# Kernel optimization log

Measured on AMD Instinct MI355X. Metric: run time of the kernel, lower is better.

The kernel has to match this reference:

```python
import jax, jax.numpy as jnp
import numpy as np

N = 50000   # nodes
E = 800000  # edges
F = 64      # num_node_features
H = 64      # hidden_channels
NB = 3      # num_blocks
G = 64      # graphs in batch
C = 10      # num_classes
EPS = 1e-5  # BatchNorm eps


def setup_inputs() -> dict:
    key = jax.random.key(0)
    ks = jax.random.split(key, 24)
    x = jax.random.normal(ks[0], (N, F), dtype=jnp.float32)
    edge_index = jax.random.randint(ks[1], (2, E), 0, N, dtype=jnp.int64)
    batch = jnp.sort(jax.random.randint(ks[2], (N,), 0, G, dtype=jnp.int64))
    s = 0.05
    inp = {
        "x": x, "edge_index": edge_index, "batch": batch,
        "pre_w": jax.random.normal(ks[3], (F, H)) * s,
        "pre_b": jnp.zeros((H,), jnp.float32),
        # stacked per-block params (blocks are structurally identical)
        "blk_prelu1": jnp.full((NB,), 0.25, jnp.float32),
        "blk_bn_gamma": jnp.ones((NB, H), jnp.float32),
        "blk_bn_beta": jnp.zeros((NB, H), jnp.float32),
        "blk_w1": jax.random.normal(ks[4], (NB, H, 2 * H)) * s,
        "blk_b1": jnp.zeros((NB, 2 * H), jnp.float32),
        "blk_prelu2": jnp.full((NB,), 0.25, jnp.float32),
        "blk_w2": jax.random.normal(ks[5], (NB, 2 * H, H)) * s,
        "blk_b2": jnp.zeros((NB, H), jnp.float32),
        "post_bn_gamma": jnp.ones((H,), jnp.float32),
        "post_bn_beta": jnp.zeros((H,), jnp.float32),
        "fc1_w": jax.random.normal(ks[6], (H, 4 * H)) * s,
        "fc1_b": jnp.zeros((4 * H,), jnp.float32),
        "post_prelu": jnp.asarray(0.25, jnp.float32),
        "fc2_w": jax.random.normal(ks[7], (4 * H, C)) * s,
        "fc2_b": jnp.zeros((C,), jnp.float32),
    }
    return inp


def _prelu(x, a):
    return jnp.where(x >= 0, x, a * x)


def _batchnorm(x, gamma, beta):
    # training-mode BN over the node dimension (biased variance), as in torch
    mean = jnp.mean(x, axis=0)
    var = jnp.var(x, axis=0)
    return (x - mean) * jax.lax.rsqrt(var + EPS) * gamma + beta


def _gcn_conv(x, W, bias, src, dst):
    # PyG GCNConv: linear transform, then D^-1/2 (A+I) D^-1/2 aggregation, then bias.
    h = x @ W                                   # [N, out]
    deg = jax.ops.segment_sum(jnp.ones((E,), h.dtype), dst, num_segments=N) + 1.0
    dinv = jax.lax.rsqrt(deg)                   # [N]
    norm = dinv[src] * dinv[dst]                # [E]
    agg = jax.ops.segment_sum(h[src] * norm[:, None], dst, num_segments=N)
    agg = agg + h * (dinv * dinv)[:, None]      # self-loop contribution
    return agg + bias


def reference(x, edge_index, batch, pre_w, pre_b,
              blk_prelu1, blk_bn_gamma, blk_bn_beta, blk_w1, blk_b1,
              blk_prelu2, blk_w2, blk_b2,
              post_bn_gamma, post_bn_beta, fc1_w, fc1_b, post_prelu, fc2_w, fc2_b):
    src, dst = edge_index[0], edge_index[1]
    h = x @ pre_w + pre_b                       # [N, H]
    for i in range(NB):
        h = _prelu(h, blk_prelu1[i])
        h = _batchnorm(h, blk_bn_gamma[i], blk_bn_beta[i])
        h = _gcn_conv(h, blk_w1[i], blk_b1[i], src, dst)   # [N, 2H]
        h = _prelu(h, blk_prelu2[i])
        h = _gcn_conv(h, blk_w2[i], blk_b2[i], src, dst)   # [N, H]
    # global mean pool per graph
    sums = jax.ops.segment_sum(h, batch, num_segments=G)   # [G, H]
    cnts = jax.ops.segment_sum(jnp.ones((N,), h.dtype), batch, num_segments=G)
    pooled = sums / jnp.maximum(cnts, 1.0)[:, None]
    out = _batchnorm(pooled, post_bn_gamma, post_bn_beta)
    out = out @ fc1_w + fc1_b
    out = _prelu(out, post_prelu)
    # dropout with p=0.0 is identity
    out = out @ fc2_w + fc2_b                   # [G, C]
    return out
```

## Files before the change

kernel.cpp:

```cpp
#include <hip/hip_runtime.h>
#include <hip/hip_fp16.h>

#define NN 50000
#define NE 800000
#define NG 64
#define NC 10
#define BN_EPS 1e-5f
#define NSB 196

typedef __attribute__((ext_vector_type(2))) _Float16 h2v;
typedef __attribute__((ext_vector_type(8))) _Float16 f16x8;
typedef __attribute__((ext_vector_type(4))) float f32x4;

__device__ __forceinline__ float2 up2(unsigned u) {
    __half2 h = *reinterpret_cast<__half2*>(&u);
    return __half22float2(h);
}
__device__ __forceinline__ unsigned pk2(float a, float b) {
    __half2 h = __floats2half2_rn(a, b);
    return *reinterpret_cast<unsigned*>(&h);
}
__device__ __forceinline__ float fdot2u(unsigned a, unsigned b, float c) {
    return __builtin_amdgcn_fdot2(__builtin_bit_cast(h2v, a), __builtin_bit_cast(h2v, b), c, false);
}


__global__ void deg_count_kernel(const int* __restrict__ dst, int* __restrict__ deg,
                                 unsigned short* __restrict__ pos16) {
    int e = blockIdx.x * blockDim.x + threadIdx.x;
    if (e < NE) {
        int d = __builtin_nontemporal_load(&dst[e]);
        unsigned short p = (unsigned short)atomicAdd(&deg[d], 1);
        __builtin_nontemporal_store(p, &pos16[e]);
    }
}

__global__ __launch_bounds__(256) void block_sum_kernel(const int* __restrict__ deg,
                                                        int* __restrict__ bsum) {
    int b = blockIdx.x, t = threadIdx.x;
    int n = b * 256 + t;
    int v = (n < NN) ? deg[n] : 0;
    __shared__ int red[256];
    red[t] = v;
    __syncthreads();
    for (int off = 128; off > 0; off >>= 1) {
        if (t < off) red[t] += red[t + off];
        __syncthreads();
    }
    if (t == 0) bsum[b] = red[0];
}

__global__ __launch_bounds__(256) void bsum_scan_kernel(const int* __restrict__ bsum,
                                                        int* __restrict__ boff) {
    __shared__ int s[256];
    int t = threadIdx.x;
    int v = (t < NSB) ? bsum[t] : 0;
    s[t] = v;
    __syncthreads();
    for (int off = 1; off < 256; off <<= 1) {
        int cur = s[t];
        int add = (t >= off) ? s[t - off] : 0;
        __syncthreads();
        s[t] = cur + add;
        __syncthreads();
    }
    if (t < NSB) boff[t] = s[t] - v;
}

__global__ __launch_bounds__(256) void csr_setup_kernel(const int* __restrict__ deg,
                                                        const int* __restrict__ boff,
                                                        int* __restrict__ row_off,
                                                        float* __restrict__ dinv,
                                                        float* __restrict__ rdeg) {
    int b = blockIdx.x, t = threadIdx.x;
    int n = b * 256 + t;
    int v = (n < NN) ? deg[n] : 0;
    __shared__ int s[256];
    s[t] = v;
    __syncthreads();
    for (int off = 1; off < 256; off <<= 1) {
        int cur = s[t];
        int add = (t >= off) ? s[t - off] : 0;
        __syncthreads();
        s[t] = cur + add;
        __syncthreads();
    }
    int excl = s[t] - v + boff[b];
    if (n < NN) {
        row_off[n] = excl;
        float d = (float)v + 1.0f;
        dinv[n] = rsqrtf(d);
        rdeg[n] = sqrtf(d);
    }
    if (n == NN - 1) row_off[NN] = NE;
}

__global__ void scatter_pass_kernel(const int* __restrict__ src, const int* __restrict__ dst,
                                    const unsigned short* __restrict__ pos16,
                                    const int* __restrict__ row_off,
                                    int* __restrict__ csr_src, int d0, int d1) {
    int e = blockIdx.x * blockDim.x + threadIdx.x;
    if (e >= NE) return;
    int d = __builtin_nontemporal_load(&dst[e]);
    if (d < d0 || d >= d1) return;
    int s = __builtin_nontemporal_load(&src[e]);
    int p = (int)__builtin_nontemporal_load(&pos16[e]);
    csr_src[row_off[d] + p] = s;
}

__global__ void arow_kernel(const int* __restrict__ row_off, const int* __restrict__ csr_src,
                            const float* __restrict__ dinv, float* __restrict__ arow) {
    int n = blockIdx.x * 256 + threadIdx.x;
    if (n >= NN) return;
    float dv = dinv[n];
    float s = dv;
    int e0 = row_off[n], e1 = row_off[n + 1];
    for (int i = e0; i < e1; ++i) s += dinv[csr_src[i]];
    arow[n] = dv * s;
}


__global__ __launch_bounds__(256) void bn_stats_kernel(const __half* __restrict__ h,
                                                       const float* __restrict__ rdeg,
                                                       const float* __restrict__ alpha_p,
                                                       float* __restrict__ stats) {
    float alpha = alpha_p[0];
    int tid = threadIdx.x;
    int c4 = (tid & 15) * 4;
    int rg = tid >> 4;
    float sx = 0, sy = 0, sz = 0, sw = 0;
    float qx = 0, qy = 0, qz = 0, qw = 0;
    for (int n = blockIdx.x * 16 + rg; n < NN; n += gridDim.x * 16) {
        float rd = rdeg[n];
        uint2 u = *(const uint2*)&h[(size_t)n * 64 + c4];
        float2 lo = up2(u.x), hi = up2(u.y);
        float a = lo.x >= 0.f ? lo.x : alpha * lo.x;
        float b = lo.y >= 0.f ? lo.y : alpha * lo.y;
        float c = hi.x >= 0.f ? hi.x : alpha * hi.x;
        float d = hi.y >= 0.f ? hi.y : alpha * hi.y;
        a *= rd; b *= rd; c *= rd; d *= rd;
        sx += a; sy += b; sz += c; sw += d;
        qx += a * a; qy += b * b; qz += c * c; qw += d * d;
    }
    __shared__ float ls[256 * 8];
    float* p = &ls[tid * 8];
    p[0] = sx; p[1] = sy; p[2] = sz; p[3] = sw;
    p[4] = qx; p[5] = qy; p[6] = qz; p[7] = qw;
    __syncthreads();
    if (tid < 128) {
        int cidx = tid >> 3;
        int j = tid & 7;
        float acc = 0.f;
        for (int r = 0; r < 16; ++r) acc += ls[(r * 16 + cidx) * 8 + j];
        int ch = cidx * 4 + (j & 3);
        if (j < 4) atomicAdd(&stats[ch], acc);
        else       atomicAdd(&stats[64 + ch], acc);
    }
}


template <bool PRELU, int OUT>
__global__ __launch_bounds__(256) void gather_kernel(const int* __restrict__ row_off,
                                                     const int* __restrict__ csr_src,
                                                     const float* __restrict__ dinv,
                                                     const float* __restrict__ bias,
                                                     const float* __restrict__ alpha_p,
                                                     const __half* __restrict__ hh,
                                                     __half* __restrict__ outp) {
    int tid = threadIdx.x;
    int r = blockIdx.x * 32 + (tid >> 3);
    int c = (tid & 7) * 8;
    if (r >= NN) return;
    float alpha = 0.f;
    if constexpr (PRELU) alpha = alpha_p[0];
    float acc[8];
    {
        uint4 u0 = *(const uint4*)&hh[(size_t)r * 64 + c];
        float2 p0 = up2(u0.x), p1 = up2(u0.y), p2 = up2(u0.z), p3 = up2(u0.w);
        acc[0] = p0.x; acc[1] = p0.y; acc[2] = p1.x; acc[3] = p1.y;
        acc[4] = p2.x; acc[5] = p2.y; acc[6] = p3.x; acc[7] = p3.y;
        if constexpr (PRELU) {
#pragma unroll
            for (int k = 0; k < 8; ++k) acc[k] = acc[k] >= 0.f ? acc[k] : alpha * acc[k];
        }
    }
    int beg = row_off[r];
    int end = row_off[r + 1];
    int nct = (end - beg + 7) >> 3;
    int base = beg;
    int q[8];
    if (nct > 0) {
#pragma unroll
        for (int j = 0; j < 8; ++j) {
            int pos = base + j;
            q[j] = csr_src[pos < end ? pos : end - 1];
        }
    }
    for (int it = 0; it < nct; ++it) {
        int s[8];
#pragma unroll
        for (int j = 0; j < 8; ++j) s[j] = q[j];
        int cbase = base;
        base += 8;
        if (it + 1 < nct) {
#pragma unroll
            for (int j = 0; j < 8; ++j) {
                int pos = base + j;
                q[j] = csr_src[pos < end ? pos : end - 1];
            }
        }
        uint4 v[8];
#pragma unroll
        for (int j = 0; j < 8; ++j) v[j] = *(const uint4*)&hh[(size_t)s[j] * 64 + c];
#pragma unroll
        for (int j = 0; j < 8; ++j) {
            float m = (cbase + j < end) ? 1.f : 0.f;
            float2 p0 = up2(v[j].x), p1 = up2(v[j].y), p2 = up2(v[j].z), p3 = up2(v[j].w);
            float e[8] = {p0.x, p0.y, p1.x, p1.y, p2.x, p2.y, p3.x, p3.y};
            if constexpr (PRELU) {
#pragma unroll
                for (int k = 0; k < 8; ++k) e[k] = e[k] >= 0.f ? e[k] : alpha * e[k];
            }
#pragma unroll
            for (int k = 0; k < 8; ++k) acc[k] = fmaf(e[k], m, acc[k]);
        }
    }
    float dv = dinv[r];
    float o[8];
    if constexpr (OUT == 2) {
#pragma unroll
        for (int k = 0; k < 8; ++k) o[k] = dv * acc[k];
    } else {
        float4 b0 = *(const float4*)&bias[c];
        float4 b1 = *(const float4*)&bias[c + 4];
        float bl[8] = {b0.x, b0.y, b0.z, b0.w, b1.x, b1.y, b1.z, b1.w};
#pragma unroll
        for (int k = 0; k < 8; ++k) o[k] = dv * acc[k] + bl[k];
        if constexpr (OUT == 1) {
#pragma unroll
            for (int k = 0; k < 8; ++k) o[k] *= dv;
        }
    }
    uint4 ov;
    ov.x = pk2(o[0], o[1]);
    ov.y = pk2(o[2], o[3]);
    ov.z = pk2(o[4], o[5]);
    ov.w = pk2(o[6], o[7]);
    *(uint4*)&outp[(size_t)r * 64 + c] = ov;
}


__global__ __launch_bounds__(256) void gemm_pre_kernel(const float* __restrict__ Af,
                                                       const float* __restrict__ W,
                                                       __half* __restrict__ outp,
                                                       const float* __restrict__ bias,
                                                       const float* __restrict__ dinv) {
    constexpr int K = 64, M = 64, BM = 128;
    constexpr int CG = M / 8;
    constexpr int RG = 256 / CG;
    constexpr int KP = K / 2;
    __shared__ unsigned Wh[KP * M];
    __shared__ unsigned Ahs[BM][KP + 4];
    int tid = threadIdx.x;
    for (int i = tid; i < KP * M; i += 256) {
        int kp = i / M, j = i % M;
        Wh[i] = pk2(W[(2 * kp) * M + j], W[(2 * kp + 1) * M + j]);
    }
    int r0 = blockIdx.x * BM;
    for (int i = tid; i < BM * (K / 4); i += 256) {
        int row = i / (K / 4);
        int k4 = (i % (K / 4)) * 4;
        int rr = r0 + row;
        if (rr > NN - 1) rr = NN - 1;
        float4 v = *(const float4*)&Af[(size_t)rr * K + k4];
        uint2 o;
        o.x = pk2(v.x, v.y);
        o.y = pk2(v.z, v.w);
        *(uint2*)&Ahs[row][k4 >> 1] = o;
    }
    __syncthreads();
    int cg = tid % CG, rg = tid / CG;
    int c = cg * 8;
    float acc[4][8];
#pragma unroll
    for (int r = 0; r < 4; ++r)
#pragma unroll
        for (int j = 0; j < 8; ++j) acc[r][j] = 0.f;
#pragma unroll 4
    for (int kp = 0; kp < KP; kp += 2) {
        uint2 a2[4];
#pragma unroll
        for (int r = 0; r < 4; ++r) a2[r] = *(const uint2*)&Ahs[rg + r * RG][kp];
#pragma unroll
        for (int kk = 0; kk < 2; ++kk) {
            const unsigned* wp = &Wh[(kp + kk) * M + c];
            uint4 w0 = *(const uint4*)wp;
            uint4 w1 = *(const uint4*)(wp + 4);
#pragma unroll
            for (int r = 0; r < 4; ++r) {
                unsigned av = kk ? a2[r].y : a2[r].x;
                acc[r][0] = fdot2u(av, w0.x, acc[r][0]);
                acc[r][1] = fdot2u(av, w0.y, acc[r][1]);
                acc[r][2] = fdot2u(av, w0.z, acc[r][2]);
                acc[r][3] = fdot2u(av, w0.w, acc[r][3]);
                acc[r][4] = fdot2u(av, w1.x, acc[r][4]);
                acc[r][5] = fdot2u(av, w1.y, acc[r][5]);
                acc[r][6] = fdot2u(av, w1.z, acc[r][6]);
                acc[r][7] = fdot2u(av, w1.w, acc[r][7]);
            }
        }
    }
    float4 b0 = *(const float4*)&bias[c];
    float4 b1 = *(const float4*)&bias[c + 4];
#pragma unroll
    for (int r = 0; r < 4; ++r) {
        int row = r0 + rg + r * RG;
        if (row < NN) {
            float sc = dinv[row];
            uint4 o;
            o.x = pk2((acc[r][0] + b0.x) * sc, (acc[r][1] + b0.y) * sc);
            o.y = pk2((acc[r][2] + b0.z) * sc, (acc[r][3] + b0.w) * sc);
            o.z = pk2((acc[r][4] + b1.x) * sc, (acc[r][5] + b1.y) * sc);
            o.w = pk2((acc[r][6] + b1.z) * sc, (acc[r][7] + b1.w) * sc);
            *(uint4*)&outp[(size_t)row * M + c] = o;
        }
    }
}


__global__ __launch_bounds__(256) void mfma_mlp_kernel(__half* __restrict__ t,
                                                       const float* __restrict__ W1,
                                                       const float* __restrict__ b1,
                                                       const float* __restrict__ W2,
                                                       const float* __restrict__ alpha2_p,
                                                       const float* __restrict__ stats,
                                                       const float* __restrict__ gamma,
                                                       const float* __restrict__ beta,
                                                       const float* __restrict__ arow,
                                                       const float* __restrict__ dinv) {
    __shared__ __align__(16) char smem[45056];
    auto Wt1 = (_Float16(*)[72])smem;
    auto Wt2 = (_Float16(*)[136])smem;
    auto At  = (_Float16(*)[72])(smem + 18432);
    auto Ut  = (_Float16(*)[136])(smem + 27648);
    __shared__ float scS[64], shS[64];
    int tid = threadIdx.x;
    if (tid < 64) {
        float mean = stats[tid] * (1.0f / NN);
        float var  = stats[64 + tid] * (1.0f / NN) - mean * mean;
        float sc = gamma[tid] * rsqrtf(var + BN_EPS);
        scS[tid] = sc;
        shS[tid] = beta[tid] - mean * sc;
    }
    for (int i = tid; i < 128 * 32; i += 256) {
        int j = i & 127;
        int k2 = i >> 7;
        *(unsigned*)&Wt1[j][2 * k2] = pk2(W1[(2 * k2) * 128 + j], W1[(2 * k2 + 1) * 128 + j]);
    }
    int r0 = blockIdx.x * 64;
    for (int i = tid; i < 64 * 16; i += 256) {
        int row = i >> 4;
        int k4 = (i & 15) * 4;
        int rr = r0 + row;
        if (rr > NN - 1) rr = NN - 1;
        uint2 uu = *(const uint2*)&t[(size_t)rr * 64 + k4];
        float2 lo = up2(uu.x), hi = up2(uu.y);
        float av = arow[rr];
        float vx = lo.x * scS[k4 + 0] + shS[k4 + 0] * av;
        float vy = lo.y * scS[k4 + 1] + shS[k4 + 1] * av;
        float vz = hi.x * scS[k4 + 2] + shS[k4 + 2] * av;
        float vw = hi.y * scS[k4 + 3] + shS[k4 + 3] * av;
        *(unsigned*)&At[row][k4]     = pk2(vx, vy);
        *(unsigned*)&At[row][k4 + 2] = pk2(vz, vw);
    }
    __syncthreads();
    int w = tid >> 6;
    int l = tid & 63;
    int lr = l & 15;
    int lk = (l >> 4) * 8;
    int rloc = w * 16 + (l >> 4) * 4;
    {
        f32x4 acc[8];
#pragma unroll
        for (int ct = 0; ct < 8; ++ct) acc[ct] = (f32x4){0.f, 0.f, 0.f, 0.f};
#pragma unroll
        for (int k0 = 0; k0 < 64; k0 += 32) {
            f16x8 a = *(const f16x8*)&At[w * 16 + lr][k0 + lk];
#pragma unroll
            for (int ct = 0; ct < 8; ++ct) {
                f16x8 b = *(const f16x8*)&Wt1[ct * 16 + lr][k0 + lk];
                acc[ct] = __builtin_amdgcn_mfma_f32_16x16x32_f16(a, b, acc[ct], 0, 0, 0);
            }
        }
        float alpha = alpha2_p[0];
#pragma unroll
        for (int ct = 0; ct < 8; ++ct) {
            int col = ct * 16 + lr;
            float bb = b1[col];
#pragma unroll
            for (int r = 0; r < 4; ++r) {
                float v = acc[ct][r] + bb;
                v = v >= 0.f ? v : alpha * v;
                Ut[rloc + r][col] = (_Float16)v;
            }
        }
    }
    __syncthreads();
    for (int i = tid; i < 64 * 64; i += 256) {
        int j = i & 63;
        int k2 = i >> 6;
        *(unsigned*)&Wt2[j][2 * k2] = pk2(W2[(2 * k2) * 64 + j], W2[(2 * k2 + 1) * 64 + j]);
    }
    __syncthreads();
    {
        f32x4 acc[4];
#pragma unroll
        for (int ct = 0; ct < 4; ++ct) acc[ct] = (f32x4){0.f, 0.f, 0.f, 0.f};
#pragma unroll
        for (int k0 = 0; k0 < 128; k0 += 32) {
            f16x8 a = *(const f16x8*)&Ut[w * 16 + lr][k0 + lk];
#pragma unroll
            for (int ct = 0; ct < 4; ++ct) {
                f16x8 b = *(const f16x8*)&Wt2[ct * 16 + lr][k0 + lk];
                acc[ct] = __builtin_amdgcn_mfma_f32_16x16x32_f16(a, b, acc[ct], 0, 0, 0);
            }
        }
#pragma unroll
        for (int ct = 0; ct < 4; ++ct) {
            int col = ct * 16 + lr;
#pragma unroll
            for (int r = 0; r < 4; ++r) {
                int row = r0 + rloc + r;
                if (row < NN) t[(size_t)row * 64 + col] = __float2half(acc[ct][r] * dinv[row]);
            }
        }
    }
}


__global__ __launch_bounds__(256) void pool_seg_kernel(const __half* __restrict__ h,
                                                       const int* __restrict__ batch,
                                                       float* __restrict__ pooled) {
    int g = blockIdx.x;
    __shared__ int sbeg, send;
    int tid = threadIdx.x;
    if (tid == 0) {
        int lo = 0, hi = NN;
        while (lo < hi) { int mid = (lo + hi) >> 1; if (batch[mid] < g) lo = mid + 1; else hi = mid; }
        sbeg = lo;
        lo = 0; hi = NN;
        while (lo < hi) { int mid = (lo + hi) >> 1; if (batch[mid] < g + 1) lo = mid + 1; else hi = mid; }
        send = lo;
    }
    __syncthreads();
    int beg = sbeg, end = send;
    int c4 = (tid & 15) * 4;
    int rg = tid >> 4;
    float sx = 0, sy = 0, sz = 0, sw = 0;
    for (int n = beg + rg; n < end; n += 16) {
        uint2 u = *(const uint2*)&h[(size_t)n * 64 + c4];
        float2 lo = up2(u.x), hi = up2(u.y);
        sx += lo.x; sy += lo.y; sz += hi.x; sw += hi.y;
    }
    __shared__ float red[256 * 4];
    float* p = &red[tid * 4];
    p[0] = sx; p[1] = sy; p[2] = sz; p[3] = sw;
    __syncthreads();
    if (tid < 64) {
        int cg = tid >> 2;
        int j = tid & 3;
        float acc = 0.f;
        for (int r = 0; r < 16; ++r) acc += red[(r * 16 + cg) * 4 + j];
        float cnt = fmaxf((float)(end - beg), 1.0f);
        pooled[g * 64 + cg * 4 + j] = acc / cnt;
    }
}


__global__ __launch_bounds__(64) void head_stats_kernel(const float* __restrict__ pooled,
                                                        const float* __restrict__ gamma,
                                                        const float* __restrict__ beta,
                                                        float* __restrict__ headsc) {
    int ch = threadIdx.x;
    float s = 0.f, q = 0.f;
    for (int g = 0; g < 64; ++g) {
        float v = pooled[g * 64 + ch];
        s += v; q += v * v;
    }
    float mean = s * (1.0f / 64.0f);
    float var = q * (1.0f / 64.0f) - mean * mean;
    float sc = gamma[ch] * rsqrtf(var + BN_EPS);
    headsc[ch] = sc;
    headsc[64 + ch] = beta[ch] - mean * sc;
}

__global__ __launch_bounds__(256) void head_fc_kernel(const float* __restrict__ pooled,
                                                      const float* __restrict__ headsc,
                                                      const float* __restrict__ fc1w,
                                                      const float* __restrict__ fc1b,
                                                      const float* __restrict__ prelu_p,
                                                      const float* __restrict__ fc2w,
                                                      const float* __restrict__ fc2b,
                                                      float* __restrict__ out) {
    int g = blockIdx.x;
    int tid = threadIdx.x;
    __shared__ float pr[64];
    __shared__ float red[256];
    if (tid < 64) pr[tid] = pooled[g * 64 + tid] * headsc[tid] + headsc[64 + tid];
    __syncthreads();
    float alpha = prelu_p[0];
    float o1 = fc1b[tid];
    for (int k = 0; k < 64; ++k) o1 += pr[k] * fc1w[k * 256 + tid];
    o1 = o1 >= 0.f ? o1 : alpha * o1;
    for (int c = 0; c < NC; ++c) {
        red[tid] = o1 * fc2w[tid * NC + c];
        __syncthreads();
        for (int off = 128; off > 0; off >>= 1) {
            if (tid < off) red[tid] += red[tid + off];
            __syncthreads();
        }
        if (tid == 0) out[g * NC + c] = red[0] + fc2b[c];
        __syncthreads();
    }
}


extern "C" void kernel_launch(void* const* d_in, const int* in_sizes, int n_in,
                              void* d_out, int out_size, void* d_ws, size_t ws_size,
                              hipStream_t stream) {
    const float* x       = (const float*)d_in[0];
    const int*   ei      = (const int*)d_in[1];
    const int*   batch   = (const int*)d_in[2];
    const float* pre_w   = (const float*)d_in[3];
    const float* pre_b   = (const float*)d_in[4];
    const float* bp1     = (const float*)d_in[5];
    const float* bng     = (const float*)d_in[6];
    const float* bnb     = (const float*)d_in[7];
    const float* bw1     = (const float*)d_in[8];
    const float* bb1     = (const float*)d_in[9];
    const float* bp2     = (const float*)d_in[10];
    const float* bw2     = (const float*)d_in[11];
    const float* bb2     = (const float*)d_in[12];
    const float* pgamma  = (const float*)d_in[13];
    const float* pbeta   = (const float*)d_in[14];
    const float* fc1w    = (const float*)d_in[15];
    const float* fc1b    = (const float*)d_in[16];
    const float* pprelu  = (const float*)d_in[17];
    const float* fc2w    = (const float*)d_in[18];
    const float* fc2b    = (const float*)d_in[19];

    const int* src = ei;
    const int* dst = ei + NE;

    __half* hA16 = (__half*)d_ws;
    __half* t16  = hA16 + (size_t)NN * 64;
    float* dinv  = (float*)(t16 + (size_t)NN * 64);
    float* rdeg  = dinv + NN;
    float* arow  = rdeg + NN;
    float* stats = arow + NN;
    int*   deg   = (int*)(stats + 3 * 128);
    float* pooledg = (float*)(deg + NN);
    float* headsc  = pooledg + 64 * 64;
    int*   csr_src = (int*)(headsc + 128);
    int*   row_off = csr_src + NE;
    int*   bsum    = row_off + NN + 1;
    int*   boff    = bsum + NSB;
    unsigned short* pos16 = (unsigned short*)(boff + NSB);

    hipMemsetAsync(stats, 0, ((size_t)3 * 128 + NN) * 4, stream);

    deg_count_kernel<<<(NE + 255) / 256, 256, 0, stream>>>(dst, deg, pos16);
    block_sum_kernel<<<NSB, 256, 0, stream>>>(deg, bsum);
    bsum_scan_kernel<<<1, 256, 0, stream>>>(bsum, boff);
    csr_setup_kernel<<<NSB, 256, 0, stream>>>(deg, boff, row_off, dinv, rdeg);
    for (int p = 0; p < 2; ++p) {
        int d0 = p * 25000;
        int d1 = (p == 1) ? NN : d0 + 25000;
        scatter_pass_kernel<<<(NE + 255) / 256, 256, 0, stream>>>(
            src, dst, pos16, row_off, csr_src, d0, d1);
    }
    arow_kernel<<<(NN + 255) / 256, 256, 0, stream>>>(row_off, csr_src, dinv, arow);

    gemm_pre_kernel<<<(NN + 127) / 128, 256, 0, stream>>>(x, pre_w, hA16, pre_b, dinv);

    int ggrid = (NN + 31) / 32;
    for (int i = 0; i < 3; ++i) {
        const float* a1 = bp1 + i;
        const float* a2 = bp2 + i;
        const float* gm = bng + i * 64;
        const float* bt = bnb + i * 64;
        const float* w1 = bw1 + (size_t)i * 64 * 128;
        const float* b1 = bb1 + i * 128;
        const float* w2 = bw2 + (size_t)i * 128 * 64;
        const float* b2 = bb2 + i * 64;
        float* st = stats + i * 128;

        bn_stats_kernel<<<256, 256, 0, stream>>>(hA16, rdeg, a1, st);
        gather_kernel<true, 2><<<ggrid, 256, 0, stream>>>(
            row_off, csr_src, dinv, nullptr, a1, hA16, t16);
        mfma_mlp_kernel<<<(NN + 63) / 64, 256, 0, stream>>>(
            t16, w1, b1, w2, a2, st, gm, bt, arow, dinv);
        if (i < 2) {
            gather_kernel<false, 1><<<ggrid, 256, 0, stream>>>(
                row_off, csr_src, dinv, b2, nullptr, t16, hA16);
        } else {
            gather_kernel<false, 0><<<ggrid, 256, 0, stream>>>(
                row_off, csr_src, dinv, b2, nullptr, t16, hA16);
        }
    }

    pool_seg_kernel<<<NG, 256, 0, stream>>>(hA16, batch, pooledg);
    head_stats_kernel<<<1, 64, 0, stream>>>(pooledg, pgamma, pbeta, headsc);
    head_fc_kernel<<<NG, 256, 0, stream>>>(pooledg, headsc, fc1w, fc1b, pprelu,
                                           fc2w, fc2b, (float*)d_out);
}
```

Baseline: 336.8 us.

## Sort gather rows by degree, use MFMA for pre-GEMM, widen BN stats

Adds a degree histogram, a bin scan and a permutation kernel so that gather blocks process rows of similar in-degree together, in descending order, which reduces wavefront divergence and tail imbalance. The fdot2-based pre-projection GEMM is replaced by an MFMA 16x16x32 f16 kernel. The BN statistics kernel now reads 8 halves per thread and launches twice as many blocks. Three extra small kernel launches are added. Gathers now read output rows in permuted order, which lowers locality of the stores.

```diff
diff --git a/kernel.cpp b/kernel.cpp
--- a/kernel.cpp
+++ b/kernel.cpp
@@ -19,9 +19,6 @@
 __device__ __forceinline__ unsigned pk2(float a, float b) {
     __half2 h = __floats2half2_rn(a, b);
     return *reinterpret_cast<unsigned*>(&h);
-}
-__device__ __forceinline__ float fdot2u(unsigned a, unsigned b, float c) {
-    return __builtin_amdgcn_fdot2(__builtin_bit_cast(h2v, a), __builtin_bit_cast(h2v, b), c, false);
 }
 
 
@@ -93,6 +90,41 @@
         rdeg[n] = sqrtf(d);
     }
     if (n == NN - 1) row_off[NN] = NE;
+}
+
+
+__global__ __launch_bounds__(256) void deg_hist_kernel(const int* __restrict__ deg,
+                                                       int* __restrict__ hist) {
+    __shared__ int lh[64];
+    int t = threadIdx.x;
+    if (t < 64) lh[t] = 0;
+    __syncthreads();
+    int n = blockIdx.x * 256 + t;
+    if (n < NN) {
+        int b = deg[n];
+        if (b > 63) b = 63;
+        atomicAdd(&lh[b], 1);
+    }
+    __syncthreads();
+    if (t < 64 && lh[t]) atomicAdd(&hist[t], lh[t]);
+}
+
+__global__ __launch_bounds__(64) void bin_scan_kernel(const int* __restrict__ hist,
+                                                      int* __restrict__ cursor) {
+    int t = threadIdx.x;
+    int off = 0;
+    for (int b = t + 1; b < 64; ++b) off += hist[b];
+    cursor[t] = off;
+}
+
+__global__ __launch_bounds__(256) void perm_kernel(const int* __restrict__ deg,
+                                                   int* __restrict__ cursor,
+                                                   int* __restrict__ perm) {
+    int n = blockIdx.x * 256 + threadIdx.x;
+    if (n >= NN) return;
+    int b = deg[n];
+    if (b > 63) b = 63;
+    perm[atomicAdd(&cursor[b], 1)] = n;
 }
 
 __global__ void scatter_pass_kernel(const int* __restrict__ src, const int* __restrict__ dst,
@@ -126,41 +158,44 @@
                                                        float* __restrict__ stats) {
     float alpha = alpha_p[0];
     int tid = threadIdx.x;
-    int c4 = (tid & 15) * 4;
-    int rg = tid >> 4;
-    float sx = 0, sy = 0, sz = 0, sw = 0;
-    float qx = 0, qy = 0, qz = 0, qw = 0;
-    for (int n = blockIdx.x * 16 + rg; n < NN; n += gridDim.x * 16) {
+    int cg0 = tid & 7;
+    int c8 = cg0 * 8;
+    int rg = tid >> 3;
+    float sm[8], sq[8];
+#pragma unroll
+    for (int k = 0; k < 8; ++k) { sm[k] = 0.f; sq[k] = 0.f; }
+    for (int n = blockIdx.x * 32 + rg; n < NN; n += gridDim.x * 32) {
         float rd = rdeg[n];
-        uint2 u = *(const uint2*)&h[(size_t)n * 64 + c4];
-        float2 lo = up2(u.x), hi = up2(u.y);
-        float a = lo.x >= 0.f ? lo.x : alpha * lo.x;
-        float b = lo.y >= 0.f ? lo.y : alpha * lo.y;
-        float c = hi.x >= 0.f ? hi.x : alpha * hi.x;
-        float d = hi.y >= 0.f ? hi.y : alpha * hi.y;
-        a *= rd; b *= rd; c *= rd; d *= rd;
-        sx += a; sy += b; sz += c; sw += d;
-        qx += a * a; qy += b * b; qz += c * c; qw += d * d;
-    }
-    __shared__ float ls[256 * 8];
-    float* p = &ls[tid * 8];
-    p[0] = sx; p[1] = sy; p[2] = sz; p[3] = sw;
-    p[4] = qx; p[5] = qy; p[6] = qz; p[7] = qw;
+        uint4 u = *(const uint4*)&h[(size_t)n * 64 + c8];
+        float2 p0 = up2(u.x), p1 = up2(u.y), p2 = up2(u.z), p3 = up2(u.w);
+        float e[8] = {p0.x, p0.y, p1.x, p1.y, p2.x, p2.y, p3.x, p3.y};
+#pragma unroll
+        for (int k = 0; k < 8; ++k) {
+            float a = e[k] >= 0.f ? e[k] : alpha * e[k];
+            a *= rd;
+            sm[k] += a;
+            sq[k] += a * a;
+        }
+    }
+    __shared__ float ls[256 * 17];
+    float* p = &ls[tid * 17];
+#pragma unroll
+    for (int k = 0; k < 8; ++k) { p[k] = sm[k]; p[8 + k] = sq[k]; }
     __syncthreads();
     if (tid < 128) {
-        int cidx = tid >> 3;
-        int j = tid & 7;
+        int cg = tid >> 4;
+        int j = tid & 15;
         float acc = 0.f;
-        for (int r = 0; r < 16; ++r) acc += ls[(r * 16 + cidx) * 8 + j];
-        int ch = cidx * 4 + (j & 3);
-        if (j < 4) atomicAdd(&stats[ch], acc);
-        else       atomicAdd(&stats[64 + ch], acc);
+        for (int r = 0; r < 32; ++r) acc += ls[(r * 8 + cg) * 17 + j];
+        int ch = cg * 8 + (j & 7);
+        atomicAdd(&stats[(j < 8 ? 0 : 64) + ch], acc);
     }
 }
 
 
 template <bool PRELU, int OUT>
-__global__ __launch_bounds__(256) void gather_kernel(const int* __restrict__ row_off,
+__global__ __launch_bounds__(256) void gather_kernel(const int* __restrict__ perm,
+                                                     const int* __restrict__ row_off,
                                                      const int* __restrict__ csr_src,
                                                      const float* __restrict__ dinv,
                                                      const float* __restrict__ bias,
@@ -168,9 +203,10 @@
                                                      const __half* __restrict__ hh,
                                                      __half* __restrict__ outp) {
     int tid = threadIdx.x;
-    int r = blockIdx.x * 32 + (tid >> 3);
+    int idx = blockIdx.x * 32 + (tid >> 3);
     int c = (tid & 7) * 8;
-    if (r >= NN) return;
+    if (idx >= NN) return;
+    int r = perm[idx];
     float alpha = 0.f;
     if constexpr (PRELU) alpha = alpha_p[0];
     float acc[8];
@@ -250,79 +286,63 @@
 }
 
 
-__global__ __launch_bounds__(256) void gemm_pre_kernel(const float* __restrict__ Af,
+__global__ __launch_bounds__(256) void mfma_pre_kernel(const float* __restrict__ x,
                                                        const float* __restrict__ W,
                                                        __half* __restrict__ outp,
                                                        const float* __restrict__ bias,
                                                        const float* __restrict__ dinv) {
-    constexpr int K = 64, M = 64, BM = 128;
-    constexpr int CG = M / 8;
-    constexpr int RG = 256 / CG;
-    constexpr int KP = K / 2;
-    __shared__ unsigned Wh[KP * M];
-    __shared__ unsigned Ahs[BM][KP + 4];
+    __shared__ _Float16 At[128][72];
+    __shared__ _Float16 Wt[64][72];
     int tid = threadIdx.x;
-    for (int i = tid; i < KP * M; i += 256) {
-        int kp = i / M, j = i % M;
-        Wh[i] = pk2(W[(2 * kp) * M + j], W[(2 * kp + 1) * M + j]);
-    }
-    int r0 = blockIdx.x * BM;
-    for (int i = tid; i < BM * (K / 4); i += 256) {
-        int row = i / (K / 4);
-        int k4 = (i % (K / 4)) * 4;
+    for (int i = tid; i < 64 * 32; i += 256) {
+        int j = i & 63;
+        int k2 = i >> 6;
+        *(unsigned*)&Wt[j][2 * k2] = pk2(W[(2 * k2) * 64 + j], W[(2 * k2 + 1) * 64 + j]);
+    }
+    int r0 = blockIdx.x * 128;
+    for (int i = tid; i < 128 * 16; i += 256) {
+        int row = i >> 4;
+        int k4 = (i & 15) * 4;
         int rr = r0 + row;
         if (rr > NN - 1) rr = NN - 1;
-        float4 v = *(const float4*)&Af[(size_t)rr * K + k4];
-        uint2 o;
-        o.x = pk2(v.x, v.y);
-        o.y = pk2(v.z, v.w);
-        *(uint2*)&Ahs[row][k4 >> 1] = o;
-    }
-    __syncthreads();
-    int cg = tid % CG, rg = tid / CG;
-    int c = cg * 8;
-    float acc[4][8];
-#pragma unroll
-    for (int r = 0; r < 4; ++r)
-#pragma unroll
-        for (int j = 0; j < 8; ++j) acc[r][j] = 0.f;
-#pragma unroll 4
-    for (int kp = 0; kp < KP; kp += 2) {
-        uint2 a2[4];
-#pragma unroll
-        for (int r = 0; r < 4; ++r) a2[r] = *(const uint2*)&Ahs[rg + r * RG][kp];
-#pragma unroll
-        for (int kk = 0; kk < 2; ++kk) {
-            const unsigned* wp = &Wh[(kp + kk) * M + c];
-            uint4 w0 = *(const uint4*)wp;
-            uint4 w1 = *(const uint4*)(wp + 4);
+        float4 v = *(const float4*)&x[(size_t)rr * 64 + k4];
+        *(unsigned*)&At[row][k4]     = pk2(v.x, v.y);
+        *(unsigned*)&At[row][k4 + 2] = pk2(v.z, v.w);
+    }
+    __syncthreads();
+    int w = tid >> 6;
+    int l = tid & 63;
+    int lr = l & 15;
+    int lk = (l >> 4) * 8;
+    f32x4 acc[2][4];
+#pragma unroll
+    for (int rt = 0; rt < 2; ++rt)
+#pragma unroll
+        for (int ct = 0; ct < 4; ++ct) acc[rt][ct] = (f32x4){0.f, 0.f, 0.f, 0.f};
+#pragma unroll
+    for (int k0 = 0; k0 < 64; k0 += 32) {
+        f16x8 a0 = *(const f16x8*)&At[w * 32 + lr][k0 + lk];
+        f16x8 a1 = *(const f16x8*)&At[w * 32 + 16 + lr][k0 + lk];
+#pragma unroll
+        for (int ct = 0; ct < 4; ++ct) {
+            f16x8 b = *(const f16x8*)&Wt[ct * 16 + lr][k0 + lk];
+            acc[0][ct] = __builtin_amdgcn_mfma_f32_16x16x32_f16(a0, b, acc[0][ct], 0, 0, 0);
+            acc[1][ct] = __builtin_amdgcn_mfma_f32_16x16x32_f16(a1, b, acc[1][ct], 0, 0, 0);
+        }
+    }
+    int rowbase = r0 + w * 32 + (l >> 4) * 4;
+#pragma unroll
+    for (int rt = 0; rt < 2; ++rt) {
+#pragma unroll
+        for (int ct = 0; ct < 4; ++ct) {
+            int col = ct * 16 + lr;
+            float bb = bias[col];
 #pragma unroll
             for (int r = 0; r < 4; ++r) {
-                unsigned av = kk ? a2[r].y : a2[r].x;
-                acc[r][0] = fdot2u(av, w0.x, acc[r][0]);
-                acc[r][1] = fdot2u(av, w0.y, acc[r][1]);
-                acc[r][2] = fdot2u(av, w0.z, acc[r][2]);
-                acc[r][3] = fdot2u(av, w0.w, acc[r][3]);
-                acc[r][4] = fdot2u(av, w1.x, acc[r][4]);
-                acc[r][5] = fdot2u(av, w1.y, acc[r][5]);
-                acc[r][6] = fdot2u(av, w1.z, acc[r][6]);
-                acc[r][7] = fdot2u(av, w1.w, acc[r][7]);
+                int row = rowbase + rt * 16 + r;
+                if (row < NN)
+                    outp[(size_t)row * 64 + col] = __float2half((acc[rt][ct][r] + bb) * dinv[row]);
             }
-        }
-    }
-    float4 b0 = *(const float4*)&bias[c];
-    float4 b1 = *(const float4*)&bias[c + 4];
-#pragma unroll
-    for (int r = 0; r < 4; ++r) {
-        int row = r0 + rg + r * RG;
-        if (row < NN) {
-            float sc = dinv[row];
-            uint4 o;
-            o.x = pk2((acc[r][0] + b0.x) * sc, (acc[r][1] + b0.y) * sc);
-            o.y = pk2((acc[r][2] + b0.z) * sc, (acc[r][3] + b0.w) * sc);
-            o.z = pk2((acc[r][4] + b1.x) * sc, (acc[r][5] + b1.y) * sc);
-            o.w = pk2((acc[r][6] + b1.z) * sc, (acc[r][7] + b1.w) * sc);
-            *(uint4*)&outp[(size_t)row * M + c] = o;
         }
     }
 }
@@ -559,20 +579,26 @@
     float* arow  = rdeg + NN;
     float* stats = arow + NN;
     int*   deg   = (int*)(stats + 3 * 128);
-    float* pooledg = (float*)(deg + NN);
+    int*   hist  = deg + NN;
+    float* pooledg = (float*)(hist + 64);
     float* headsc  = pooledg + 64 * 64;
     int*   csr_src = (int*)(headsc + 128);
     int*   row_off = csr_src + NE;
     int*   bsum    = row_off + NN + 1;
     int*   boff    = bsum + NSB;
-    unsigned short* pos16 = (unsigned short*)(boff + NSB);
-
-    hipMemsetAsync(stats, 0, ((size_t)3 * 128 + NN) * 4, stream);
+    int*   bcur    = boff + NSB;
+    int*   perm    = bcur + 64;
+    unsigned short* pos16 = (unsigned short*)(perm + NN);
+
+    hipMemsetAsync(stats, 0, ((size_t)3 * 128 + NN + 64) * 4, stream);
 
     deg_count_kernel<<<(NE + 255) / 256, 256, 0, stream>>>(dst, deg, pos16);
     block_sum_kernel<<<NSB, 256, 0, stream>>>(deg, bsum);
     bsum_scan_kernel<<<1, 256, 0, stream>>>(bsum, boff);
     csr_setup_kernel<<<NSB, 256, 0, stream>>>(deg, boff, row_off, dinv, rdeg);
+    deg_hist_kernel<<<NSB, 256, 0, stream>>>(deg, hist);
+    bin_scan_kernel<<<1, 64, 0, stream>>>(hist, bcur);
+    perm_kernel<<<NSB, 256, 0, stream>>>(deg, bcur, perm);
     for (int p = 0; p < 2; ++p) {
         int d0 = p * 25000;
         int d1 = (p == 1) ? NN : d0 + 25000;
@@ -581,7 +607,7 @@
     }
     arow_kernel<<<(NN + 255) / 256, 256, 0, stream>>>(row_off, csr_src, dinv, arow);
 
-    gemm_pre_kernel<<<(NN + 127) / 128, 256, 0, stream>>>(x, pre_w, hA16, pre_b, dinv);
+    mfma_pre_kernel<<<(NN + 127) / 128, 256, 0, stream>>>(x, pre_w, hA16, pre_b, dinv);
 
     int ggrid = (NN + 31) / 32;
     for (int i = 0; i < 3; ++i) {
@@ -595,17 +621,17 @@
         const float* b2 = bb2 + i * 64;
         float* st = stats + i * 128;
 
-        bn_stats_kernel<<<256, 256, 0, stream>>>(hA16, rdeg, a1, st);
+        bn_stats_kernel<<<512, 256, 0, stream>>>(hA16, rdeg, a1, st);
         gather_kernel<true, 2><<<ggrid, 256, 0, stream>>>(
-            row_off, csr_src, dinv, nullptr, a1, hA16, t16);
+            perm, row_off, csr_src, dinv, nullptr, a1, hA16, t16);
         mfma_mlp_kernel<<<(NN + 63) / 64, 256, 0, stream>>>(
             t16, w1, b1, w2, a2, st, gm, bt, arow, dinv);
         if (i < 2) {
             gather_kernel<false, 1><<<ggrid, 256, 0, stream>>>(
-                row_off, csr_src, dinv, b2, nullptr, t16, hA16);
+                perm, row_off, csr_src, dinv, b2, nullptr, t16, hA16);
         } else {
             gather_kernel<false, 0><<<ggrid, 256, 0, stream>>>(
-                row_off, csr_src, dinv, b2, nullptr, t16, hA16);
+                perm, row_off, csr_src, dinv, b2, nullptr, t16, hA16);
         }
     }
 
```

Measured after the change: 493.6 us. 1.47x slower.
